# Kernel tuning notes

Hardware: AMD Instinct MI355X
Metric: run time of the kernel (lower is better)

Reference implementation:

```python
import jax, jax.numpy as jnp
import numpy as np

K = 1000   # grid rows (detections from model 1, truncated to 1000)
N = 1000   # grid cols (detections from model 2)
M = 900000 # number of non-empty (overlapping) pairs
F = 7      # per-pair feature dim
SENTINEL = -9999.0


def setup_inputs() -> dict:
    key = jax.random.key(0)
    ks = jax.random.split(key, 12)
    def w(k, o, i):
        return jax.random.normal(k, (o, i), dtype=jnp.float32) * 0.05
    def b(k, o):
        return jax.random.normal(k, (o,), dtype=jnp.float32) * 0.05
    return {
        "input_1": jax.random.normal(ks[0], (1, F, 1, M), dtype=jnp.float32),
        "T_out": jnp.zeros((1, K, N), dtype=jnp.float32),
        "T_indices": jax.random.randint(ks[1], (2, M), 0, K),
        "w1": w(ks[2], 18, F),  "b1": b(ks[3], 18),
        "w2": w(ks[4], 36, 18), "b2": b(ks[5], 36),
        "w3": w(ks[6], 36, 36), "b3": b(ks[7], 36),
        "w4": w(ks[8], 1, 36),  "b4": b(ks[9], 1),
    }


def reference(input_1, T_out, T_indices, w1, b1, w2, b2, w3, b3, w4, b4):
    # 1x1 conv stack == channel matmuls on the flattened [F, M] features.
    x = input_1[0, :, 0, :]                       # [F, M]
    h = jax.nn.relu(w1 @ x + b1[:, None])         # [18, M]
    h = jax.nn.relu(w2 @ h + b2[:, None])         # [36, M]
    h = jax.nn.relu(w3 @ h + b3[:, None])         # [36, M]
    vals = (w4 @ h + b4[:, None])[0]              # [M]

    grid = jnp.full(T_out.shape, SENTINEL, dtype=T_out.dtype)  # [1, K, N]
    grid = grid.at[:, T_indices[0], T_indices[1]].set(vals[None, :])

    # MaxPool2d([1, N]) -> max over cols; MaxPool2d([K, 1]) -> max over rows.
    row_max = grid.max(axis=2).squeeze()          # [K]
    col_max = grid.max(axis=1).squeeze()          # [N]
    return (row_max, col_max)
```

## Files before the change

### kernel.cpp

```cpp
#include <hip/hip_runtime.h>
#include <stdint.h>

#define KK 1000
#define NN 1000
#define MM 900000
#define FF 7
#define SENTINEL -9999.0f

template <int N, typename F>
__device__ __forceinline__ void unroll_loop(F&& f) {
    if constexpr (N > 0) {
        unroll_loop<N - 1>(static_cast<F&&>(f));
        f(N - 1);
    }
}

__global__ __launch_bounds__(256) void init_grid(ulonglong2* __restrict__ g, int n2,
                                                 float* __restrict__ outcol) {
    int i = blockIdx.x * 256 + threadIdx.x;
    if (i < n2) g[i] = make_ulonglong2(0ULL, 0ULL);
    if (i < NN) outcol[i] = SENTINEL;
}

__global__ __launch_bounds__(256, 3) void mlp_scatter(
    const float* __restrict__ in,
    const int*   __restrict__ idx,
    const float* __restrict__ w1, const float* __restrict__ b1,
    const float* __restrict__ w2, const float* __restrict__ b2,
    const float* __restrict__ w3, const float* __restrict__ b3,
    const float* __restrict__ w4, const float* __restrict__ b4,
    unsigned long long* __restrict__ grid)
{
    int t = blockIdx.x * 256 + threadIdx.x;
    int m0 = t * 2;
    if (m0 >= MM) return;

    float xa[FF], xb[FF];
    unroll_loop<FF>([&](int f) {
        float2 v = *reinterpret_cast<const float2*>(in + (size_t)f * MM + m0);
        xa[f] = v.x; xb[f] = v.y;
    });

    float h1a[18], h1b[18];
    unroll_loop<18>([&](int o) {
        float a = b1[o], b = a;
        unroll_loop<FF>([&](int i) {
            float w_ = w1[o * FF + i];
            a = fmaf(w_, xa[i], a); b = fmaf(w_, xb[i], b);
        });
        h1a[o] = fmaxf(a, 0.0f); h1b[o] = fmaxf(b, 0.0f);
    });

    float h2a[36], h2b[36];
    unroll_loop<36>([&](int o) {
        float a = b2[o], b = a;
        unroll_loop<18>([&](int i) {
            float w_ = w2[o * 18 + i];
            a = fmaf(w_, h1a[i], a); b = fmaf(w_, h1b[i], b);
        });
        h2a[o] = fmaxf(a, 0.0f); h2b[o] = fmaxf(b, 0.0f);
    });

    float va = b4[0], vb = va;
    unroll_loop<36>([&](int o) {
        float a = b3[o], b = a;
        unroll_loop<36>([&](int i) {
            float w_ = w3[o * 36 + i];
            a = fmaf(w_, h2a[i], a); b = fmaf(w_, h2b[i], b);
        });
        float w4o = w4[o];
        va = fmaf(w4o, fmaxf(a, 0.0f), va);
        vb = fmaf(w4o, fmaxf(b, 0.0f), vb);
    });

    int2 rr = *reinterpret_cast<const int2*>(idx + m0);
    int2 cc = *reinterpret_cast<const int2*>(idx + MM + m0);
    unsigned long long pa =
        ((unsigned long long)(unsigned)(m0 + 1) << 32) | (unsigned)__float_as_uint(va);
    unsigned long long pb =
        ((unsigned long long)(unsigned)(m0 + 2) << 32) | (unsigned)__float_as_uint(vb);
    atomicMax(&grid[rr.x * NN + cc.x], pa);
    atomicMax(&grid[rr.y * NN + cc.y], pb);
}

#define CCHUNKS 25
#define CROWS   (KK / CCHUNKS)

__global__ __launch_bounds__(256) void maxes(const unsigned long long* __restrict__ g,
                                             float* __restrict__ out) {
    int b = blockIdx.x;
    if (b < KK) {
        int r = b;
        float mx = SENTINEL;
        for (int c = threadIdx.x; c < NN; c += 256) {
            unsigned long long p = g[(size_t)r * NN + c];
            if (p) mx = fmaxf(mx, __uint_as_float((unsigned)p));
        }
        __shared__ float red[256];
        red[threadIdx.x] = mx;
        __syncthreads();
        for (int s = 128; s > 0; s >>= 1) {
            if (threadIdx.x < s)
                red[threadIdx.x] = fmaxf(red[threadIdx.x], red[threadIdx.x + s]);
            __syncthreads();
        }
        if (threadIdx.x == 0) out[r] = red[0];
    } else {
        int cb = b - KK;
        int n  = (cb & 3) * 256 + (int)threadIdx.x;
        if (n < NN) {
            int k0 = (cb >> 2) * CROWS;
            float mx = SENTINEL;
            for (int k = k0; k < k0 + CROWS; ++k) {
                unsigned long long p = g[(size_t)k * NN + n];
                if (p) mx = fmaxf(mx, __uint_as_float((unsigned)p));
            }
            atomicMax(out + KK + n, mx);
        }
    }
}

extern "C" void kernel_launch(void* const* d_in, const int* in_sizes, int n_in,
                              void* d_out, int out_size, void* d_ws, size_t ws_size,
                              hipStream_t stream) {
    const float* in  = (const float*)d_in[0];
    const int*   idx = (const int*)d_in[2];
    const float* w1  = (const float*)d_in[3];
    const float* b1  = (const float*)d_in[4];
    const float* w2  = (const float*)d_in[5];
    const float* b2  = (const float*)d_in[6];
    const float* w3  = (const float*)d_in[7];
    const float* b3  = (const float*)d_in[8];
    const float* w4  = (const float*)d_in[9];
    const float* b4  = (const float*)d_in[10];

    unsigned long long* grid = (unsigned long long*)d_ws;
    float* out = (float*)d_out;

    const int n2 = (KK * NN) / 2;
    init_grid<<<(n2 + 255) / 256, 256, 0, stream>>>((ulonglong2*)grid, n2, out + KK);

    mlp_scatter<<<(MM / 2 + 255) / 256, 256, 0, stream>>>(
        in, idx, w1, b1, w2, b2, w3, b3, w4, b4, grid);

    maxes<<<KK + 100, 256, 0, stream>>>(grid, out);
}
```

Before: 184.9 us.

## Use packed fp16 dot2 for MLP layers 2-3 with pre-converted weights

Converts the first two hidden-layer activations to packed fp16 and runs layers 2 and 3 with v_dot2 (fp16 inputs, fp32 accumulation), using fp16 weight copies prepared by a new prep kernel that also zeroes the grid. This roughly halves the FMA instruction count and the register footprint, which allows the occupancy hint to rise from 3 to 4 waves. The column-max pass is also split into more chunks. The cost is reduced precision in the hidden activations and weights, so the outputs may differ slightly from the fp32 reference.

```diff
diff --git a/kernel.cpp b/kernel.cpp
--- a/kernel.cpp
+++ b/kernel.cpp
@@ -6,6 +6,9 @@
 #define MM 900000
 #define FF 7
 #define SENTINEL -9999.0f
+
+typedef _Float16 h2v __attribute__((ext_vector_type(2)));
+typedef __fp16  h2f __attribute__((ext_vector_type(2)));
 
 template <int N, typename F>
 __device__ __forceinline__ void unroll_loop(F&& f) {
@@ -15,19 +18,61 @@
     }
 }
 
-__global__ __launch_bounds__(256) void init_grid(ulonglong2* __restrict__ g, int n2,
-                                                 float* __restrict__ outcol) {
-    int i = blockIdx.x * 256 + threadIdx.x;
-    if (i < n2) g[i] = make_ulonglong2(0ULL, 0ULL);
-    if (i < NN) outcol[i] = SENTINEL;
-}
-
-__global__ __launch_bounds__(256, 3) void mlp_scatter(
+#if __has_builtin(__builtin_amdgcn_fdot2)
+__device__ __forceinline__ float dot2(h2v a, h2v b, float c) {
+    return __builtin_amdgcn_fdot2(__builtin_bit_cast(h2f, a),
+                                  __builtin_bit_cast(h2f, b), c, false);
+}
+#else
+__device__ __forceinline__ float dot2(h2v a, h2v b, float c) {
+    return fmaf((float)a.x, (float)b.x, fmaf((float)a.y, (float)b.y, c));
+}
+#endif
+
+__device__ __forceinline__ h2v pkrtz(float a, float b) {
+#if __has_builtin(__builtin_amdgcn_cvt_pkrtz)
+    return __builtin_bit_cast(h2v, __builtin_amdgcn_cvt_pkrtz(a, b));
+#else
+    return h2v{(_Float16)a, (_Float16)b};
+#endif
+}
+
+#define ZB ((KK * NN / 2 + 255) / 256)
+#define SB 4
+
+__global__ __launch_bounds__(256) void prep(
+    ulonglong2* __restrict__ g, float* __restrict__ outcol,
+    const float* __restrict__ w2, const float* __restrict__ w3,
+    h2v* __restrict__ w2h, h2v* __restrict__ w3h)
+{
+    int b = blockIdx.x;
+    if (b < ZB) {
+        int i = b * 256 + threadIdx.x;
+        if (i < KK * NN / 2) g[i] = make_ulonglong2(0ULL, 0ULL);
+    } else if (b < ZB + SB) {
+        int i = (b - ZB) * 256 + threadIdx.x;
+        if (i < NN) outcol[i] = SENTINEL;
+    } else {
+        int t = threadIdx.x;
+        for (int p = t; p < 36 * 9; p += 256) {
+            int o = p / 9, ip = p - o * 9;
+            w2h[p] = h2v{(_Float16)w2[o * 18 + 2 * ip],
+                         (_Float16)w2[o * 18 + 2 * ip + 1]};
+        }
+        for (int p = t; p < 36 * 18; p += 256) {
+            int o = p / 18, ip = p - o * 18;
+            w3h[p] = h2v{(_Float16)w3[o * 36 + 2 * ip],
+                         (_Float16)w3[o * 36 + 2 * ip + 1]};
+        }
+    }
+}
+
+__global__ __launch_bounds__(256, 4) void mlp_scatter(
     const float* __restrict__ in,
     const int*   __restrict__ idx,
     const float* __restrict__ w1, const float* __restrict__ b1,
-    const float* __restrict__ w2, const float* __restrict__ b2,
-    const float* __restrict__ w3, const float* __restrict__ b3,
+    const h2v*   __restrict__ w2h, const float* __restrict__ b2,
+    const h2v*   __restrict__ w3h, const float* __restrict__ b3,
     const float* __restrict__ w4, const float* __restrict__ b4,
     unsigned long long* __restrict__ grid)
 {
@@ -35,42 +80,50 @@
     int m0 = t * 2;
     if (m0 >= MM) return;
 
-    float xa[FF], xb[FF];
+    float2 x[FF];
     unroll_loop<FF>([&](int f) {
-        float2 v = *reinterpret_cast<const float2*>(in + (size_t)f * MM + m0);
-        xa[f] = v.x; xb[f] = v.y;
-    });
-
-    float h1a[18], h1b[18];
-    unroll_loop<18>([&](int o) {
-        float a = b1[o], b = a;
+        x[f] = *reinterpret_cast<const float2*>(in + (size_t)f * MM + m0);
+    });
+
+    h2v h1a[9], h1b[9];
+    unroll_loop<9>([&](int p) {
+        float a0 = b1[2 * p], a1 = b1[2 * p + 1];
+        float c0 = a0, c1 = a1;
         unroll_loop<FF>([&](int i) {
-            float w_ = w1[o * FF + i];
-            a = fmaf(w_, xa[i], a); b = fmaf(w_, xb[i], b);
+            float w0 = w1[(2 * p) * FF + i];
+            float w1_ = w1[(2 * p + 1) * FF + i];
+            a0 = fmaf(w0, x[i].x, a0);  c0 = fmaf(w0, x[i].y, c0);
+            a1 = fmaf(w1_, x[i].x, a1); c1 = fmaf(w1_, x[i].y, c1);
         });
-        h1a[o] = fmaxf(a, 0.0f); h1b[o] = fmaxf(b, 0.0f);
-    });
-
-    float h2a[36], h2b[36];
-    unroll_loop<36>([&](int o) {
-        float a = b2[o], b = a;
-        unroll_loop<18>([&](int i) {
-            float w_ = w2[o * 18 + i];
-            a = fmaf(w_, h1a[i], a); b = fmaf(w_, h1b[i], b);
+        h1a[p] = pkrtz(fmaxf(a0, 0.0f), fmaxf(a1, 0.0f));
+        h1b[p] = pkrtz(fmaxf(c0, 0.0f), fmaxf(c1, 0.0f));
+    });
+
+    h2v h2a[18], h2b[18];
+    unroll_loop<18>([&](int p) {
+        float a0 = b2[2 * p], a1 = b2[2 * p + 1];
+        float c0 = a0, c1 = a1;
+        unroll_loop<9>([&](int ip) {
+            h2v w0 = w2h[(2 * p) * 9 + ip];
+            h2v w1_ = w2h[(2 * p + 1) * 9 + ip];
+            a0 = dot2(w0, h1a[ip], a0);  c0 = dot2(w0, h1b[ip], c0);
+            a1 = dot2(w1_, h1a[ip], a1); c1 = dot2(w1_, h1b[ip], c1);
         });
-        h2a[o] = fmaxf(a, 0.0f); h2b[o] = fmaxf(b, 0.0f);
+        h2a[p] = pkrtz(fmaxf(a0, 0.0f), fmaxf(a1, 0.0f));
+        h2b[p] = pkrtz(fmaxf(c0, 0.0f), fmaxf(c1, 0.0f));
     });
 
     float va = b4[0], vb = va;
     unroll_loop<36>([&](int o) {
-        float a = b3[o], b = a;
-        unroll_loop<36>([&](int i) {
-            float w_ = w3[o * 36 + i];
-            a = fmaf(w_, h2a[i], a); b = fmaf(w_, h2b[i], b);
+        float a = b3[o], c = a;
+        unroll_loop<18>([&](int ip) {
+            h2v w = w3h[o * 18 + ip];
+            a = dot2(w, h2a[ip], a);
+            c = dot2(w, h2b[ip], c);
         });
         float w4o = w4[o];
         va = fmaf(w4o, fmaxf(a, 0.0f), va);
-        vb = fmaf(w4o, fmaxf(b, 0.0f), vb);
+        vb = fmaf(w4o, fmaxf(c, 0.0f), vb);
     });
 
     int2 rr = *reinterpret_cast<const int2*>(idx + m0);
@@ -83,8 +136,8 @@
     atomicMax(&grid[rr.y * NN + cc.y], pb);
 }
 
-#define CCHUNKS 25
-#define CROWS   (KK / CCHUNKS)
+#define CCH 50
+#define CR  (KK / CCH)
 
 __global__ __launch_bounds__(256) void maxes(const unsigned long long* __restrict__ g,
                                              float* __restrict__ out) {
@@ -109,9 +162,9 @@
         int cb = b - KK;
         int n  = (cb & 3) * 256 + (int)threadIdx.x;
         if (n < NN) {
-            int k0 = (cb >> 2) * CROWS;
+            int k0 = (cb >> 2) * CR;
             float mx = SENTINEL;
-            for (int k = k0; k < k0 + CROWS; ++k) {
+            for (int k = k0; k < k0 + CR; ++k) {
                 unsigned long long p = g[(size_t)k * NN + n];
                 if (p) mx = fmaxf(mx, __uint_as_float((unsigned)p));
             }
@@ -135,13 +188,14 @@
     const float* b4  = (const float*)d_in[10];
 
     unsigned long long* grid = (unsigned long long*)d_ws;
-    float* out = (float*)d_out;
-
-    const int n2 = (KK * NN) / 2;
-    init_grid<<<(n2 + 255) / 256, 256, 0, stream>>>((ulonglong2*)grid, n2, out + KK);
+    h2v* w2h = (h2v*)((char*)d_ws + 8000000);
+    h2v* w3h = (h2v*)((char*)d_ws + 8001312);
+    float* out  = (float*)d_out;
+
+    prep<<<ZB + SB + 1, 256, 0, stream>>>((ulonglong2*)grid, out + KK, w2, w3, w2h, w3h);
 
     mlp_scatter<<<(MM / 2 + 255) / 256, 256, 0, stream>>>(
-        in, idx, w1, b1, w2, b2, w3, b3, w4, b4, grid);
-
-    maxes<<<KK + 100, 256, 0, stream>>>(grid, out);
-}
+        in, idx, w1, b1, w2h, b2, w3h, b3, w4, b4, grid);
+
+    maxes<<<KK + 4 * CCH, 256, 0, stream>>>(grid, out);
+}
```

Result: faster. 164.5 us (-11.1%).

## Run MLP layers 2-3 on fp16 MFMA with LDS-staged weights and activations

Applied to the files above, without the earlier changes.

Replaces the per-thread scalar FMA evaluation of the 18->36 and 36->36 layers with fp16 MFMA 16x16x32 instructions. Weights and per-wave activations are staged in LDS as fp16, and each thread now handles one pair instead of two. The final reduction uses cross-lane shuffles. Grid zeroing and the column-output init are split into separate blocks, and the column-max chunking changes from 25 to 50. The fp16 conversion of activations and weights reduces precision, which can perturb the max values and the last-write tie ordering.

```diff
diff --git a/kernel.cpp b/kernel.cpp
--- a/kernel.cpp
+++ b/kernel.cpp
@@ -7,6 +7,9 @@
 #define FF 7
 #define SENTINEL -9999.0f
 
+typedef __fp16 f16x8 __attribute__((ext_vector_type(8)));
+typedef float  f32x4 __attribute__((ext_vector_type(4)));
+
 template <int N, typename F>
 __device__ __forceinline__ void unroll_loop(F&& f) {
     if constexpr (N > 0) {
@@ -15,12 +18,32 @@
     }
 }
 
-__global__ __launch_bounds__(256) void init_grid(ulonglong2* __restrict__ g, int n2,
-                                                 float* __restrict__ outcol) {
-    int i = blockIdx.x * 256 + threadIdx.x;
-    if (i < n2) g[i] = make_ulonglong2(0ULL, 0ULL);
-    if (i < NN) outcol[i] = SENTINEL;
-}
+__device__ __forceinline__ unsigned pk2(float a, float b) {
+    return __builtin_bit_cast(unsigned, __builtin_amdgcn_cvt_pkrtz(a, b));
+}
+
+#define ZB ((KK * NN / 2 + 255) / 256)
+#define SB 4
+
+__global__ __launch_bounds__(256) void prep(ulonglong2* __restrict__ g,
+                                            float* __restrict__ outcol) {
+    int b = blockIdx.x;
+    if (b < ZB) {
+        int i = b * 256 + threadIdx.x;
+        if (i < KK * NN / 2) g[i] = make_ulonglong2(0ULL, 0ULL);
+    } else {
+        int i = (b - ZB) * 256 + threadIdx.x;
+        if (i < NN) outcol[i] = SENTINEL;
+    }
+}
+
+#define W2_OFF  0
+#define W3_OFF  3840
+#define W4_OFF  10752
+#define B2_OFF  10944
+#define B3_OFF  11136
+#define ACT_OFF 11328
+#define LDS_BYTES (ACT_OFF + 4 * 9216)
 
 __global__ __launch_bounds__(256, 3) void mlp_scatter(
     const float* __restrict__ in,
@@ -31,60 +54,120 @@
     const float* __restrict__ w4, const float* __restrict__ b4,
     unsigned long long* __restrict__ grid)
 {
-    int t = blockIdx.x * 256 + threadIdx.x;
-    int m0 = t * 2;
-    if (m0 >= MM) return;
-
-    float xa[FF], xb[FF];
-    unroll_loop<FF>([&](int f) {
-        float2 v = *reinterpret_cast<const float2*>(in + (size_t)f * MM + m0);
-        xa[f] = v.x; xb[f] = v.y;
-    });
-
-    float h1a[18], h1b[18];
-    unroll_loop<18>([&](int o) {
-        float a = b1[o], b = a;
+    __shared__ __align__(16) char smem[LDS_BYTES];
+    const int t = threadIdx.x;
+
+    for (int i = t; i < LDS_BYTES / 16; i += 256)
+        ((uint4*)smem)[i] = make_uint4(0, 0, 0, 0);
+    __syncthreads();
+
+    for (int i = t; i < 36 * 18; i += 256) {
+        int r = i / 18, k = i - r * 18;
+        ((__fp16*)(smem + W2_OFF + r * 80))[k] = (__fp16)w2[i];
+    }
+    for (int i = t; i < 36 * 36; i += 256) {
+        int r = i / 36, k = i - r * 36;
+        ((__fp16*)(smem + W3_OFF + r * 144))[k] = (__fp16)w3[i];
+    }
+    if (t < 36) {
+        ((float*)(smem + W4_OFF))[t] = w4[t];
+        ((float*)(smem + B2_OFF))[t] = b2[t];
+        ((float*)(smem + B3_OFF))[t] = b3[t];
+    }
+    __syncthreads();
+
+    const int wave = t >> 6, l = t & 63;
+    const int g = l >> 4, li = l & 15;
+    char* act = smem + ACT_OFF + wave * 9216;
+    const int mbase = blockIdx.x * 256 + wave * 64;
+    if (mbase >= MM) return;
+
+    const int m = mbase + l;
+    const int mc = m < MM ? m : MM - 1;
+    float x[FF];
+    unroll_loop<FF>([&](int f) { x[f] = in[(size_t)f * MM + mc]; });
+
+    unsigned hw[9];
+    unroll_loop<9>([&](int p) {
+        float a = b1[2 * p], b = b1[2 * p + 1];
         unroll_loop<FF>([&](int i) {
-            float w_ = w1[o * FF + i];
-            a = fmaf(w_, xa[i], a); b = fmaf(w_, xb[i], b);
+            a = fmaf(w1[(2 * p) * FF + i], x[i], a);
+            b = fmaf(w1[(2 * p + 1) * FF + i], x[i], b);
         });
-        h1a[o] = fmaxf(a, 0.0f); h1b[o] = fmaxf(b, 0.0f);
-    });
-
-    float h2a[36], h2b[36];
-    unroll_loop<36>([&](int o) {
-        float a = b2[o], b = a;
-        unroll_loop<18>([&](int i) {
-            float w_ = w2[o * 18 + i];
-            a = fmaf(w_, h1a[i], a); b = fmaf(w_, h1b[i], b);
+        hw[p] = pk2(fmaxf(a, 0.0f), fmaxf(b, 0.0f));
+    });
+    {
+        char* row = act + l * 144;
+        *(uint4*)(row)      = make_uint4(hw[0], hw[1], hw[2], hw[3]);
+        *(uint4*)(row + 16) = make_uint4(hw[4], hw[5], hw[6], hw[7]);
+        *(uint2*)(row + 32) = make_uint2(hw[8], 0u);
+    }
+
+    const f32x4 zf = {0.f, 0.f, 0.f, 0.f};
+
+    f16x8 a2[3], bq[4];
+    unroll_loop<3>([&](int T) {
+        a2[T] = *(const f16x8*)(smem + W2_OFF + (16 * T + li) * 80 + g * 16);
+    });
+    unroll_loop<4>([&](int q) {
+        bq[q] = *(const f16x8*)(act + (16 * q + li) * 144 + g * 16);
+    });
+    f32x4 b2v[3];
+    unroll_loop<3>([&](int T) {
+        b2v[T] = *(const f32x4*)(smem + B2_OFF + (16 * T + 4 * g) * 4);
+    });
+    f32x4 acc[3][4];
+    unroll_loop<3>([&](int T) { unroll_loop<4>([&](int q) {
+        acc[T][q] = __builtin_amdgcn_mfma_f32_16x16x32_f16(a2[T], bq[q], zf, 0, 0, 0);
+    }); });
+    unroll_loop<3>([&](int T) { unroll_loop<4>([&](int q) {
+        f32x4 d = acc[T][q];
+        unsigned lo = pk2(fmaxf(d[0] + b2v[T][0], 0.0f), fmaxf(d[1] + b2v[T][1], 0.0f));
+        unsigned hi = pk2(fmaxf(d[2] + b2v[T][2], 0.0f), fmaxf(d[3] + b2v[T][3], 0.0f));
+        *(uint2*)(act + (16 * q + li) * 144 + (16 * T + 4 * g) * 2) = make_uint2(lo, hi);
+    }); });
+
+    f16x8 a3[3][2];
+    unroll_loop<3>([&](int T) { unroll_loop<2>([&](int s) {
+        a3[T][s] = *(const f16x8*)(smem + W3_OFF + (16 * T + li) * 144 + s * 64 + g * 16);
+    }); });
+    f32x4 wv[3], b3v[3];
+    unroll_loop<3>([&](int T) {
+        wv[T]  = *(const f32x4*)(smem + W4_OFF + (16 * T + 4 * g) * 4);
+        b3v[T] = *(const f32x4*)(smem + B3_OFF + (16 * T + 4 * g) * 4);
+    });
+    float vfin = 0.0f;
+    unroll_loop<4>([&](int q) {
+        const char* brow = act + (16 * q + li) * 144;
+        f16x8 bb0 = *(const f16x8*)(brow + g * 16);
+        f16x8 bb1 = *(const f16x8*)(brow + 64 + g * 16);
+        float s = 0.0f;
+        unroll_loop<3>([&](int T) {
+            f32x4 c = __builtin_amdgcn_mfma_f32_16x16x32_f16(a3[T][0], bb0, zf, 0, 0, 0);
+            c = __builtin_amdgcn_mfma_f32_16x16x32_f16(a3[T][1], bb1, c, 0, 0, 0);
+            s += wv[T][0] * fmaxf(c[0] + b3v[T][0], 0.0f)
+               + wv[T][1] * fmaxf(c[1] + b3v[T][1], 0.0f)
+               + wv[T][2] * fmaxf(c[2] + b3v[T][2], 0.0f)
+               + wv[T][3] * fmaxf(c[3] + b3v[T][3], 0.0f);
         });
-        h2a[o] = fmaxf(a, 0.0f); h2b[o] = fmaxf(b, 0.0f);
-    });
-
-    float va = b4[0], vb = va;
-    unroll_loop<36>([&](int o) {
-        float a = b3[o], b = a;
-        unroll_loop<36>([&](int i) {
-            float w_ = w3[o * 36 + i];
-            a = fmaf(w_, h2a[i], a); b = fmaf(w_, h2b[i], b);
-        });
-        float w4o = w4[o];
-        va = fmaf(w4o, fmaxf(a, 0.0f), va);
-        vb = fmaf(w4o, fmaxf(b, 0.0f), vb);
-    });
-
-    int2 rr = *reinterpret_cast<const int2*>(idx + m0);
-    int2 cc = *reinterpret_cast<const int2*>(idx + MM + m0);
-    unsigned long long pa =
-        ((unsigned long long)(unsigned)(m0 + 1) << 32) | (unsigned)__float_as_uint(va);
-    unsigned long long pb =
-        ((unsigned long long)(unsigned)(m0 + 2) << 32) | (unsigned)__float_as_uint(vb);
-    atomicMax(&grid[rr.x * NN + cc.x], pa);
-    atomicMax(&grid[rr.y * NN + cc.y], pb);
-}
-
-#define CCHUNKS 25
-#define CROWS   (KK / CCHUNKS)
+        s += __shfl_xor(s, 16);
+        s += __shfl_xor(s, 32);
+        if (g == q) vfin = s;
+    });
+
+    const int mf = mbase + 16 * g + li;
+    if (mf < MM) {
+        float v = vfin + b4[0];
+        int r = idx[mf];
+        int c = idx[MM + mf];
+        unsigned long long packed =
+            ((unsigned long long)(unsigned)(mf + 1) << 32) | (unsigned)__float_as_uint(v);
+        atomicMax(&grid[r * NN + c], packed);
+    }
+}
+
+#define CCH 50
+#define CR  (KK / CCH)
 
 __global__ __launch_bounds__(256) void maxes(const unsigned long long* __restrict__ g,
                                              float* __restrict__ out) {
@@ -109,9 +192,9 @@
         int cb = b - KK;
         int n  = (cb & 3) * 256 + (int)threadIdx.x;
         if (n < NN) {
-            int k0 = (cb >> 2) * CROWS;
+            int k0 = (cb >> 2) * CR;
             float mx = SENTINEL;
-            for (int k = k0; k < k0 + CROWS; ++k) {
+            for (int k = k0; k < k0 + CR; ++k) {
                 unsigned long long p = g[(size_t)k * NN + n];
                 if (p) mx = fmaxf(mx, __uint_as_float((unsigned)p));
             }
@@ -137,11 +220,10 @@
     unsigned long long* grid = (unsigned long long*)d_ws;
     float* out = (float*)d_out;
 
-    const int n2 = (KK * NN) / 2;
-    init_grid<<<(n2 + 255) / 256, 256, 0, stream>>>((ulonglong2*)grid, n2, out + KK);
-
-    mlp_scatter<<<(MM / 2 + 255) / 256, 256, 0, stream>>>(
+    prep<<<ZB + SB, 256, 0, stream>>>((ulonglong2*)grid, out + KK);
+
+    mlp_scatter<<<(MM + 255) / 256, 256, 0, stream>>>(
         in, idx, w1, b1, w2, b2, w3, b3, w4, b4, grid);
 
-    maxes<<<KK + 100, 256, 0, stream>>>(grid, out);
-}
+    maxes<<<KK + 4 * CCH, 256, 0, stream>>>(grid, out);
+}
```

Result: faster. 159.6 us (-13.7%).
